# Kernel optimization log

Measured on AMD Instinct MI355X. Metric: run time of the kernel, lower is better.

The kernel has to match this reference:

```python
import jax, jax.numpy as jnp
import numpy as np

N_SAMPLES, N_DET, N_UP, N_DOWN = 8192, 16, 16, 16


def setup_inputs() -> dict:
    key = jax.random.key(0)
    k1, k2, k3 = jax.random.split(key, 3)
    a = jax.random.normal(k1, (N_SAMPLES, N_DET, N_UP, N_UP), dtype=jnp.float32)
    b = jax.random.normal(k2, (N_SAMPLES, N_DET, N_DOWN, N_DOWN), dtype=jnp.float32)
    w = jax.random.normal(k3, (N_DET, 1), dtype=jnp.float32)
    return {"a": a, "b": b, "w": w}


def reference(a, b, w):
    # Batched slogdet over (n_samples, n_det) small matrices
    sign_a, logdet_a = jnp.linalg.slogdet(a)  # (n_samples, n_det)
    sign_b, logdet_b = jnp.linalg.slogdet(b)  # (n_samples, n_det)
    x = logdet_a + logdet_b                   # (n_samples, n_det)
    xmax = jnp.max(x, axis=-1, keepdims=True)  # (n_samples, 1)
    # Numerically-stabilized signed log-sum-exp combined with weights w
    shifted_exp = sign_a * sign_b * jnp.exp(x - xmax)  # (n_samples, n_det)
    shifted_sum = shifted_exp @ w                      # (n_samples, 1)
    log_psi = jnp.log(jnp.abs(shifted_sum)) + xmax     # (n_samples, 1)
    # sign(unshifted_exp @ w) == sign(shifted_sum) since exp(xmax) > 0
    sign_psi = jnp.sign(shifted_sum)                   # (n_samples, 1)
    return log_psi, sign_psi
```

## Files before the change

### kernel.cpp

```cpp
#include <hip/hip_runtime.h>
#include <math.h>

#define NDET 16
#define NDIM 16

template<int OWNER>
__device__ __forceinline__ float bcast4f(float v) {
    constexpr int ctrl = OWNER * 0x55;
    return __int_as_float(
        __builtin_amdgcn_mov_dpp(__float_as_int(v), ctrl, 0xF, 0xF, true));
}

template<int K>
__device__ __forceinline__ void qr_step(float (&c)[4][16], float &prod, float &sgn) {
    constexpr int OWNER = K & 3;
    constexpr int LC    = K >> 2;
    constexpr int JMIN  = K >> 2;

    float s0 = 0.0f, s1 = 0.0f;
    #pragma unroll
    for (int i = K; i < 16; i += 2)     s0 = fmaf(c[LC][i], c[LC][i], s0);
    #pragma unroll
    for (int i = K + 1; i < 16; i += 2) s1 = fmaf(c[LC][i], c[LC][i], s1);

    const float n2    = bcast4f<OWNER>(s0 + s1);
    const float xK    = bcast4f<OWNER>(c[LC][K]);
    const float alpha = __builtin_amdgcn_sqrtf(n2);
    const float vK    = xK + copysignf(alpha, xK);
    const float beta  = __builtin_amdgcn_rcpf(alpha * fabsf(vK));
    prod *= alpha;
    sgn = (xK < 0.0f) ? -sgn : sgn;

    float bv[16];
    bv[K] = vK;
    #pragma unroll
    for (int i = K + 1; i < 16; ++i) bv[i] = bcast4f<OWNER>(c[LC][i]);

    #pragma unroll
    for (int j = JMIN; j < 4; ++j) {
        float w0 = bv[K] * c[j][K], w1 = 0.0f;
        #pragma unroll
        for (int i = K + 1; i < 16; i += 2) w0 = fmaf(bv[i], c[j][i], w0);
        #pragma unroll
        for (int i = K + 2; i < 16; i += 2) w1 = fmaf(bv[i], c[j][i], w1);
        const float t = (w0 + w1) * beta;
        #pragma unroll
        for (int i = K; i < 16; ++i)
            c[j][i] = fmaf(-t, bv[i], c[j][i]);
    }
}

template<int K>
__device__ __forceinline__ void qr_all(float (&c)[4][16], float &prod, float &sgn) {
    qr_step<K>(c, prod, sgn);
    if constexpr (K < 14) qr_all<K + 1>(c, prod, sgn);
}

__global__ __launch_bounds__(256) void logabssumdet_kernel(
    const float* __restrict__ a,
    const float* __restrict__ b,
    const float* __restrict__ w,
    float* __restrict__ out,
    int n_samples)
{
    const int tid    = threadIdx.x;
    const int lane4  = tid & 3;
    const int group  = tid >> 2;
    const int mat_id = blockIdx.x * 64 + group;
    const int n_mats = n_samples * NDET;

    __shared__ float sx[64];
    __shared__ float ss[64];

    float x = 0.0f, sgn = 1.0f;

    if (mat_id < n_mats) {
        #pragma unroll 1
        for (int m = 0; m < 2; ++m) {
            const float* src = (m == 0) ? a : b;
            const float4* mb =
                reinterpret_cast<const float4*>(src + (size_t)mat_id * (NDIM * NDIM)) + lane4;

            float c[4][16];
            #pragma unroll
            for (int i = 0; i < 16; ++i) {
                const float4 v = mb[i * 4];
                c[0][i] = v.x; c[1][i] = v.y; c[2][i] = v.z; c[3][i] = v.w;
            }

            float prod = 1.0f;
            qr_all<0>(c, prod, sgn);
            prod *= bcast4f<3>(c[3][15]);

            x += __logf(fabsf(prod));
            sgn = (prod < 0.0f) ? -sgn : sgn;
        }
    }

    if (lane4 == 0) { sx[group] = x; ss[group] = sgn; }
    __syncthreads();

    if (tid < 4) {
        const int sample = blockIdx.x * 4 + tid;
        if (sample < n_samples) {
            const int base = tid * NDET;
            float xmax = -INFINITY;
            #pragma unroll
            for (int d = 0; d < NDET; ++d) xmax = fmaxf(xmax, sx[base + d]);
            float sum = 0.0f;
            #pragma unroll
            for (int d = 0; d < NDET; ++d)
                sum += ss[base + d] * __expf(sx[base + d] - xmax) * w[d];
            out[sample] = __logf(fabsf(sum)) + xmax;
            out[n_samples + sample] = (sum > 0.0f) ? 1.0f : ((sum < 0.0f) ? -1.0f : 0.0f);
        }
    }
}

extern "C" void kernel_launch(void* const* d_in, const int* in_sizes, int n_in,
                              void* d_out, int out_size, void* d_ws, size_t ws_size,
                              hipStream_t stream)
{
    const float* a = (const float*)d_in[0];
    const float* b = (const float*)d_in[1];
    const float* w = (const float*)d_in[2];
    float* out = (float*)d_out;

    const int n_samples = in_sizes[0] / (NDET * NDIM * NDIM);
    const int blocks = (n_samples + 3) / 4;
    logabssumdet_kernel<<<blocks, 256, 0, stream>>>(a, b, w, out, n_samples);
}
```

Before: 46.73 us.

## Software-pipeline matrix loads across QR passes and reduce per wavefront

```diff
diff --git a/kernel.cpp b/kernel.cpp
--- a/kernel.cpp
+++ b/kernel.cpp
@@ -3,6 +3,7 @@
 
 #define NDET 16
 #define NDIM 16
+#define NIT  2
 
 template<int OWNER>
 __device__ __forceinline__ float bcast4f(float v) {
@@ -63,56 +64,76 @@
     float* __restrict__ out,
     int n_samples)
 {
-    const int tid    = threadIdx.x;
-    const int lane4  = tid & 3;
-    const int group  = tid >> 2;
-    const int mat_id = blockIdx.x * 64 + group;
-    const int n_mats = n_samples * NDET;
+    const int tid   = threadIdx.x;
+    const int lane4 = tid & 3;
+    const int quad  = (tid >> 2) & 15;
+    const int wid   = tid >> 6;
+    const int s0    = (blockIdx.x * 4 + wid) * NIT;
 
-    __shared__ float sx[64];
-    __shared__ float ss[64];
+    __shared__ float sxw[4][16];
+    __shared__ float ssw[4][16];
 
-    float x = 0.0f, sgn = 1.0f;
+    float4 nxt[16];
+    {
+        const int sc = (s0 < n_samples) ? s0 : (n_samples - 1);
+        const float4* p = reinterpret_cast<const float4*>(
+            a + ((size_t)sc * NDET + quad) * (NDIM * NDIM)) + lane4;
+        #pragma unroll
+        for (int i = 0; i < 16; ++i) nxt[i] = p[i * 4];
+    }
 
-    if (mat_id < n_mats) {
+    #pragma unroll 1
+    for (int it = 0; it < NIT; ++it) {
+        const int s = s0 + it;
+        float x = 0.0f, sg = 1.0f;
+
         #pragma unroll 1
         for (int m = 0; m < 2; ++m) {
-            const float* src = (m == 0) ? a : b;
-            const float4* mb =
-                reinterpret_cast<const float4*>(src + (size_t)mat_id * (NDIM * NDIM)) + lane4;
-
             float c[4][16];
             #pragma unroll
             for (int i = 0; i < 16; ++i) {
-                const float4 v = mb[i * 4];
-                c[0][i] = v.x; c[1][i] = v.y; c[2][i] = v.z; c[3][i] = v.w;
+                c[0][i] = nxt[i].x; c[1][i] = nxt[i].y;
+                c[2][i] = nxt[i].z; c[3][i] = nxt[i].w;
             }
 
+            if (!(it == NIT - 1 && m == 1)) {
+                const float* nsrc = (m == 0) ? b : a;
+                int ns = (m == 0) ? s : (s + 1);
+                ns = (ns < n_samples) ? ns : (n_samples - 1);
+                const float4* p = reinterpret_cast<const float4*>(
+                    nsrc + ((size_t)ns * NDET + quad) * (NDIM * NDIM)) + lane4;
+                #pragma unroll
+                for (int i = 0; i < 16; ++i) nxt[i] = p[i * 4];
+            }
+            __builtin_amdgcn_sched_barrier(0);
+
             float prod = 1.0f;
-            qr_all<0>(c, prod, sgn);
+            qr_all<0>(c, prod, sg);
             prod *= bcast4f<3>(c[3][15]);
+            x += __logf(fabsf(prod));
+            sg = (prod < 0.0f) ? -sg : sg;
+        }
 
-            x += __logf(fabsf(prod));
-            sgn = (prod < 0.0f) ? -sgn : sgn;
-        }
-    }
+        if (lane4 == 0) { sxw[wid][quad] = x; ssw[wid][quad] = sg; }
+        asm volatile("s_waitcnt lgkmcnt(0)" ::: "memory");
 
-    if (lane4 == 0) { sx[group] = x; ss[group] = sgn; }
-    __syncthreads();
-
-    if (tid < 4) {
-        const int sample = blockIdx.x * 4 + tid;
-        if (sample < n_samples) {
-            const int base = tid * NDET;
+        if (s < n_samples) {
             float xmax = -INFINITY;
+            float xs[NDET], gs[NDET];
             #pragma unroll
-            for (int d = 0; d < NDET; ++d) xmax = fmaxf(xmax, sx[base + d]);
+            for (int d = 0; d < NDET; ++d) {
+                xs[d] = sxw[wid][d];
+                gs[d] = ssw[wid][d];
+                xmax  = fmaxf(xmax, xs[d]);
+            }
             float sum = 0.0f;
             #pragma unroll
             for (int d = 0; d < NDET; ++d)
-                sum += ss[base + d] * __expf(sx[base + d] - xmax) * w[d];
-            out[sample] = __logf(fabsf(sum)) + xmax;
-            out[n_samples + sample] = (sum > 0.0f) ? 1.0f : ((sum < 0.0f) ? -1.0f : 0.0f);
+                sum += gs[d] * __expf(xs[d] - xmax) * w[d];
+            if ((tid & 63) == 0) {
+                out[s] = __logf(fabsf(sum)) + xmax;
+                out[n_samples + s] = (sum > 0.0f) ? 1.0f : ((sum < 0.0f) ? -1.0f : 0.0f);
+            }
         }
     }
 }
@@ -127,6 +148,6 @@
     float* out = (float*)d_out;
 
     const int n_samples = in_sizes[0] / (NDET * NDIM * NDIM);
-    const int blocks = (n_samples + 3) / 4;
+    const int blocks = (n_samples + 4 * NIT - 1) / (4 * NIT);
     logabssumdet_kernel<<<blocks, 256, 0, stream>>>(a, b, w, out, n_samples);
 }
```

Measured after the change: 51.26 us. +9.7%, slower.
